# Optimization experiments

Measured on AMD Instinct MI355X. Metric: run time of the kernel, lower is better.

The kernel has to match this reference:

```python
import jax, jax.numpy as jnp
import numpy as np

H = 128          # hidden_size
D = 128          # input_size
N_LEAVES = 262144  # 2**18 leaves -> complete binary tree, 18 reduction levels


def setup_inputs() -> dict:
    key = jax.random.key(0)
    k1, k2, k3, k4, k5 = jax.random.split(key, 5)
    s = 0.05
    return {
        "leaf_features": jax.random.normal(k1, (N_LEAVES, D), jnp.float32),
        "W_x": jax.random.normal(k2, (D, 5 * H), jnp.float32) * s,  # torch Linear weight (transposed)
        "b_x": jax.random.normal(k3, (5 * H,), jnp.float32) * s,
        "U_L": jax.random.normal(k4, (H, 5 * H), jnp.float32) * s,  # no bias, per module
        "U_R": jax.random.normal(k5, (H, 5 * H), jnp.float32) * s,
    }


def _cell(gates, left_c=None, right_c=None):
    # gates: [n, 5H] -> chunk(5, dim=1) order: i, f_L, f_R, o, u
    i, f_L, f_R, o, u = jnp.split(gates, 5, axis=1)
    c = jax.nn.sigmoid(i) * jnp.tanh(u)
    if left_c is not None:
        c = c + jax.nn.sigmoid(f_L) * left_c
    if right_c is not None:
        c = c + jax.nn.sigmoid(f_R) * right_c
    h = jax.nn.sigmoid(o) * jnp.tanh(c)
    return h, c


def reference(leaf_features, W_x, b_x, U_L, U_R):
    # Leaves: cell(feat, None, None, None, None) -> only W_x gates, all nodes batched.
    h, c = _cell(leaf_features @ W_x + b_x)  # [N_LEAVES, H]
    # Internal nodes, processed level-by-level (depth batching of the recursion).
    # Internal x = zeros -> W_x contributes only its bias b_x.
    while h.shape[0] > 1:
        gates = b_x + h[0::2] @ U_L + h[1::2] @ U_R  # [n/2, 5H]
        h, c = _cell(gates, c[0::2], c[1::2])
    return h  # root hidden state, shape (1, H)
```

## Files before the change

kernel.cpp:

```cpp
#include <hip/hip_runtime.h>
#include <hip/hip_bf16.h>
#include <stdint.h>


#define H5 640
#define HH 128
#define NLEAF 262144

typedef __attribute__((ext_vector_type(4))) float f32x4;
typedef __attribute__((ext_vector_type(8))) short bf16x8;
typedef __attribute__((ext_vector_type(4))) unsigned int u32x4;

static __device__ __forceinline__ unsigned int f2bf(float f) {
  union { float f; unsigned int i; } v; v.f = f;
  unsigned int r = v.i + 0x7FFF + ((v.i >> 16) & 1);
  return r >> 16;
}

static __device__ __forceinline__ float sigf(float x) {
  return 1.0f / (1.0f + __expf(-x));
}
static __device__ __forceinline__ float tanh_fast(float x) {
  float t = __expf(2.0f * x);
  return (t - 1.0f) / (t + 1.0f);
}

__global__ void pack_weights(const float* __restrict__ srcA,
                             const float* __restrict__ srcB,
                             int split, int KT, unsigned short* __restrict__ dst) {
  int t = blockIdx.x * blockDim.x + threadIdx.x;
  int total = 40 * KT * 64;
  if (t >= total) return;
  int lane = t & 63;
  int kf = (t >> 6) % KT;
  int nf = (t >> 6) / KT;
  int col = nf * 16 + (lane & 15);
  int k0 = kf * 32 + (lane >> 4) * 8;
  unsigned int w[4];
#pragma unroll
  for (int p = 0; p < 4; ++p) {
    int ka = k0 + 2 * p, kb = k0 + 2 * p + 1;
    float fa = (ka < split) ? srcA[(size_t)ka * H5 + col] : srcB[(size_t)(ka - split) * H5 + col];
    float fb = (kb < split) ? srcA[(size_t)kb * H5 + col] : srcB[(size_t)(kb - split) * H5 + col];
    w[p] = f2bf(fa) | (f2bf(fb) << 16);
  }
  u32x4 v; unsigned int* vp = (unsigned int*)&v;
  vp[0] = w[0]; vp[1] = w[1]; vp[2] = w[2]; vp[3] = w[3];
  *((u32x4*)(dst + (size_t)t * 8)) = v;
}

__global__ void cast_leaf(const float* __restrict__ src,
                          unsigned short* __restrict__ dst, long n8) {
  long t = (long)blockIdx.x * blockDim.x + threadIdx.x;
  if (t >= n8) return;
  const float4* s = (const float4*)src + t * 2;
  float4 x = s[0], y = s[1];
  u32x4 v; unsigned int* vp = (unsigned int*)&v;
  vp[0] = f2bf(x.x) | (f2bf(x.y) << 16);
  vp[1] = f2bf(x.z) | (f2bf(x.w) << 16);
  vp[2] = f2bf(y.x) | (f2bf(y.y) << 16);
  vp[3] = f2bf(y.z) | (f2bf(y.w) << 16);
  *((u32x4*)(dst + t * 8)) = v;
}

template <int KT, bool HAS_C>
__global__ __launch_bounds__(256, 4) void level_fused(
    const unsigned short* __restrict__ A,
    const unsigned short* __restrict__ Bpk,
    const float* __restrict__ bx,
    const float* __restrict__ c_child,
    unsigned short* __restrict__ h_out,
    float* __restrict__ c_out,
    float* __restrict__ h_f32_out,
    int n, int NT) {
  constexpr int K = KT * 32;
  __shared__ unsigned short smemB[5 * KT * 512];
  const int lane = threadIdx.x & 63;
  const int wid = threadIdx.x >> 6;
  const int by = blockIdx.y;

  for (int e = wid; e < 5 * KT; e += 4) {
    int g = e / KT, kt = e % KT;
    const u32x4* src =
        (const u32x4*)(Bpk + ((size_t)((g * 8 + by) * KT + kt) * 512) + lane * 8);
    *((u32x4*)(smemB + e * 512 + lane * 8)) = *src;
  }
  __syncthreads();

  const int jc = by * 16 + (lane & 15);
  float bxv[5];
#pragma unroll
  for (int g = 0; g < 5; ++g) bxv[g] = bx[g * 128 + jc];

  const int kch = (lane >> 4) * 8;

  for (int t = blockIdx.x; t < NT; t += gridDim.x) {
    const int r0 = t * 256 + wid * 64 + (lane & 15);
    f32x4 acc[4][5];
#pragma unroll
    for (int m = 0; m < 4; ++m)
#pragma unroll
      for (int g = 0; g < 5; ++g) acc[m][g] = (f32x4)0.0f;

#pragma unroll 2
    for (int kt = 0; kt < KT; ++kt) {
      bf16x8 a[4];
#pragma unroll
      for (int m = 0; m < 4; ++m)
        a[m] = *(const bf16x8*)(A + (size_t)(r0 + m * 16) * K + kt * 32 + kch);
#pragma unroll
      for (int g = 0; g < 5; ++g) {
        bf16x8 b = *(const bf16x8*)(smemB + (g * KT + kt) * 512 + lane * 8);
#pragma unroll
        for (int m = 0; m < 4; ++m)
          acc[m][g] = __builtin_amdgcn_mfma_f32_16x16x32_bf16(a[m], b, acc[m][g], 0, 0, 0);
      }
    }

#pragma unroll
    for (int m = 0; m < 4; ++m) {
      const int ib = t * 256 + wid * 64 + m * 16 + (lane >> 4) * 4;
#pragma unroll
      for (int reg = 0; reg < 4; ++reg) {
        const int i = ib + reg;
        if (i >= n) continue;
        float gi = acc[m][0][reg] + bxv[0];
        float go = acc[m][3][reg] + bxv[3];
        float gu = acc[m][4][reg] + bxv[4];
        float c = sigf(gi) * tanh_fast(gu);
        if (HAS_C) {
          float gfL = acc[m][1][reg] + bxv[1];
          float gfR = acc[m][2][reg] + bxv[2];
          float cL = c_child[(size_t)(2 * i) * HH + jc];
          float cR = c_child[(size_t)(2 * i + 1) * HH + jc];
          c += sigf(gfL) * cL + sigf(gfR) * cR;
        }
        float h = sigf(go) * tanh_fast(c);
        h_out[(size_t)i * HH + jc] = (unsigned short)f2bf(h);
        c_out[(size_t)i * HH + jc] = c;
        if (h_f32_out) h_f32_out[(size_t)i * HH + jc] = h;
      }
    }
  }
}

extern "C" void kernel_launch(void* const* d_in, const int* in_sizes, int n_in,
                              void* d_out, int out_size, void* d_ws, size_t ws_size,
                              hipStream_t stream) {
  const float* leaf = (const float*)d_in[0];
  const float* Wx = (const float*)d_in[1];
  const float* bx = (const float*)d_in[2];
  const float* UL = (const float*)d_in[3];
  const float* UR = (const float*)d_in[4];
  float* out = (float*)d_out;

  char* ws = (char*)d_ws;
  size_t off = 0;
  auto alloc = [&](size_t bytes) -> void* {
    void* p = ws + off;
    off += (bytes + 1023) & ~(size_t)1023;
    return p;
  };
  unsigned short* Wx_pk = (unsigned short*)alloc((size_t)40 * 4 * 64 * 8 * 2);
  unsigned short* U_pk = (unsigned short*)alloc((size_t)40 * 8 * 64 * 8 * 2);
  unsigned short* leaf_bf = (unsigned short*)alloc((size_t)NLEAF * HH * 2);
  unsigned short* hA = (unsigned short*)alloc((size_t)NLEAF * HH * 2);
  unsigned short* hB = (unsigned short*)alloc((size_t)(NLEAF / 2) * HH * 2);
  float* cA = (float*)alloc((size_t)NLEAF * HH * 4);
  float* cB = (float*)alloc((size_t)(NLEAF / 2) * HH * 4);

  pack_weights<<<(40 * 4 * 64 + 255) / 256, 256, 0, stream>>>(Wx, Wx, 128, 4, Wx_pk);
  pack_weights<<<(40 * 8 * 64 + 255) / 256, 256, 0, stream>>>(UL, UR, 128, 8, U_pk);
  long n8 = (long)NLEAF * HH / 8;
  cast_leaf<<<(unsigned)(n8 / 256), 256, 0, stream>>>(leaf, leaf_bf, n8);

  level_fused<4, false><<<dim3(128, 8), 256, 0, stream>>>(
      leaf_bf, Wx_pk, bx, nullptr, hA, cA, nullptr, NLEAF, NLEAF / 256);

  unsigned short* hs[2] = {hA, hB};
  float* cs[2] = {cA, cB};
  int cur = 0;
  int n = NLEAF / 2;
  for (int lvl = 1; lvl <= 18; ++lvl) {
    float* f32out = (lvl == 18) ? out : nullptr;
    int NT = (n + 255) / 256;
    int gx = NT < 128 ? NT : 128;
    level_fused<8, true><<<dim3(gx, 8), 256, 0, stream>>>(
        hs[cur], U_pk, bx, cs[cur], hs[cur ^ 1], cs[cur ^ 1], f32out, n, NT);
    cur ^= 1;
    n >>= 1;
  }
  (void)in_sizes; (void)n_in; (void)out_size; (void)ws_size;
}
```

Measured before the change: 787.2 us.

## Store cell state column-major so child c loads and stores vectorize

Result: no change. 786.1 us (-0.1%).

```diff
diff --git a/kernel.cpp b/kernel.cpp
--- a/kernel.cpp
+++ b/kernel.cpp
@@ -63,7 +63,7 @@
   *((u32x4*)(dst + t * 8)) = v;
 }
 
-template <int KT, bool HAS_C>
+template <int KT, bool HAS_C, bool WRITE_F32>
 __global__ __launch_bounds__(256, 4) void level_fused(
     const unsigned short* __restrict__ A,
     const unsigned short* __restrict__ Bpk,
@@ -72,7 +72,7 @@
     unsigned short* __restrict__ h_out,
     float* __restrict__ c_out,
     float* __restrict__ h_f32_out,
-    int n, int NT) {
+    int n, int NT, int ldr, int ldw) {
   constexpr int K = KT * 32;
   __shared__ unsigned short smemB[5 * KT * 512];
   const int lane = threadIdx.x & 63;
@@ -117,13 +117,23 @@
       }
     }
 
+    const int ib0 = t * 256 + wid * 64 + (lane >> 4) * 4;
+    f32x4 cva[4], cvb[4];
+    if (HAS_C) {
+#pragma unroll
+      for (int m = 0; m < 4; ++m) {
+        const float* p = c_child + (size_t)jc * ldr + 2 * (ib0 + m * 16);
+        cva[m] = *(const f32x4*)p;
+        cvb[m] = *(const f32x4*)(p + 4);
+      }
+    }
 #pragma unroll
     for (int m = 0; m < 4; ++m) {
-      const int ib = t * 256 + wid * 64 + m * 16 + (lane >> 4) * 4;
+      const int ibm = ib0 + m * 16;
+      f32x4 cst;
 #pragma unroll
       for (int reg = 0; reg < 4; ++reg) {
-        const int i = ib + reg;
-        if (i >= n) continue;
+        const int i = ibm + reg;
         float gi = acc[m][0][reg] + bxv[0];
         float go = acc[m][3][reg] + bxv[3];
         float gu = acc[m][4][reg] + bxv[4];
@@ -131,15 +141,19 @@
         if (HAS_C) {
           float gfL = acc[m][1][reg] + bxv[1];
           float gfR = acc[m][2][reg] + bxv[2];
-          float cL = c_child[(size_t)(2 * i) * HH + jc];
-          float cR = c_child[(size_t)(2 * i + 1) * HH + jc];
+          float cL = (reg < 2) ? cva[m][2 * reg] : cvb[m][2 * (reg - 2)];
+          float cR = (reg < 2) ? cva[m][2 * reg + 1] : cvb[m][2 * (reg - 2) + 1];
           c += sigf(gfL) * cL + sigf(gfR) * cR;
         }
-        float h = sigf(go) * tanh_fast(c);
-        h_out[(size_t)i * HH + jc] = (unsigned short)f2bf(h);
-        c_out[(size_t)i * HH + jc] = c;
-        if (h_f32_out) h_f32_out[(size_t)i * HH + jc] = h;
+        cst[reg] = c;
+        if (i < n) {
+          float h = sigf(go) * tanh_fast(c);
+          h_out[(size_t)i * HH + jc] = (unsigned short)f2bf(h);
+          if (WRITE_F32) h_f32_out[(size_t)i * HH + jc] = h;
+        }
       }
+      if (ibm < n)
+        *((f32x4*)(c_out + (size_t)jc * ldw + ibm)) = cst;
     }
   }
 }
@@ -161,6 +175,8 @@
     off += (bytes + 1023) & ~(size_t)1023;
     return p;
   };
+  auto ldof = [](int n) { return n < 4 ? 4 : n; };
+
   unsigned short* Wx_pk = (unsigned short*)alloc((size_t)40 * 4 * 64 * 8 * 2);
   unsigned short* U_pk = (unsigned short*)alloc((size_t)40 * 8 * 64 * 8 * 2);
   unsigned short* leaf_bf = (unsigned short*)alloc((size_t)NLEAF * HH * 2);
@@ -174,19 +190,26 @@
   long n8 = (long)NLEAF * HH / 8;
   cast_leaf<<<(unsigned)(n8 / 256), 256, 0, stream>>>(leaf, leaf_bf, n8);
 
-  level_fused<4, false><<<dim3(128, 8), 256, 0, stream>>>(
-      leaf_bf, Wx_pk, bx, nullptr, hA, cA, nullptr, NLEAF, NLEAF / 256);
+  level_fused<4, false, false><<<dim3(128, 8), 256, 0, stream>>>(
+      leaf_bf, Wx_pk, bx, nullptr, hA, cA, nullptr, NLEAF, NLEAF / 256, 0, NLEAF);
 
   unsigned short* hs[2] = {hA, hB};
   float* cs[2] = {cA, cB};
   int cur = 0;
   int n = NLEAF / 2;
   for (int lvl = 1; lvl <= 18; ++lvl) {
-    float* f32out = (lvl == 18) ? out : nullptr;
     int NT = (n + 255) / 256;
     int gx = NT < 128 ? NT : 128;
-    level_fused<8, true><<<dim3(gx, 8), 256, 0, stream>>>(
-        hs[cur], U_pk, bx, cs[cur], hs[cur ^ 1], cs[cur ^ 1], f32out, n, NT);
+    int ldr = ldof(2 * n), ldw = ldof(n);
+    if (lvl < 18) {
+      level_fused<8, true, false><<<dim3(gx, 8), 256, 0, stream>>>(
+          hs[cur], U_pk, bx, cs[cur], hs[cur ^ 1], cs[cur ^ 1], nullptr,
+          n, NT, ldr, ldw);
+    } else {
+      level_fused<8, true, true><<<dim3(gx, 8), 256, 0, stream>>>(
+          hs[cur], U_pk, bx, cs[cur], hs[cur ^ 1], cs[cur ^ 1], out,
+          n, NT, ldr, ldw);
+    }
     cur ^= 1;
     n >>= 1;
   }
```
